# Performance work log

Hardware: AMD Instinct MI355X
Metric: run time of the kernel (lower is better)

Reference implementation:

```python
import jax, jax.numpy as jnp
import numpy as np
import math

L, D, NH, DFF, RPE = 6, 256, 8, 1024, 512
HD = D // NH
B, NQ = 2, 300
FH, FW = 64, 64
N = FH * FW
STRIDE = 16
SCALE = 1.0 / math.sqrt(HD)


def _ln(x, w, b, eps=1e-5):
    m = jnp.mean(x, -1, keepdims=True)
    v = jnp.mean((x - m) ** 2, -1, keepdims=True)
    return (x - m) * jax.lax.rsqrt(v + eps) * w + b


def _mha_self(x, pos, in_w, in_b, out_w, out_b):
    # torch nn.MultiheadAttention with packed in_proj, q=k=x+pos, v=x
    qk = x + pos
    wq, wk, wv = jnp.split(in_w, 3, 0)
    bq, bk, bv = jnp.split(in_b, 3, 0)
    q = (qk @ wq.T + bq).reshape(B, NQ, NH, HD)
    k = (qk @ wk.T + bk).reshape(B, NQ, NH, HD)
    v = (x @ wv.T + bv).reshape(B, NQ, NH, HD)
    a = jax.nn.softmax(jnp.einsum('bqhd,bkhd->bhqk', q, k) * SCALE, -1)
    o = jnp.einsum('bhqk,bkhd->bqhd', a, v).reshape(B, NQ, D)
    return o @ out_w.T + out_b


def _cross(q_in, box, k_in, v_in, qw, qb, kw, kb, vw, vb, pw, pb,
           c1w1, c1b1, c1w2, c2w1, c2b1, c2w2):
    # box: [B,NQ,1,4] xyxy in absolute pixels; learned relative position bias
    pos_x = (jnp.arange(FW, dtype=jnp.float32) + 0.5) * STRIDE  # linspace(0.5,w-0.5,w)*stride
    pos_y = (jnp.arange(FH, dtype=jnp.float32) + 0.5) * STRIDE
    dx = box[..., 0::2] - pos_x[None, None, :, None]  # [B,NQ,FW,2]
    dy = box[..., 1::2] - pos_y[None, None, :, None]  # [B,NQ,FH,2]
    rpe_x = jax.nn.relu(dx @ c1w1.T + c1b1) @ c1w2.T  # [B,NQ,FW,NH]
    rpe_y = jax.nn.relu(dy @ c2w1.T + c2b1) @ c2w2.T  # [B,NQ,FH,NH]
    rpe = (rpe_y[:, :, :, None, :] + rpe_x[:, :, None, :, :]).reshape(B, NQ, N, NH)
    q = ((q_in @ qw.T + qb) * SCALE).reshape(B, NQ, NH, HD)
    k = (k_in @ kw.T + kb).reshape(B, N, NH, HD)
    v = (v_in @ vw.T + vb).reshape(B, N, NH, HD)
    attn = jnp.einsum('bqhd,bkhd->bhqk', q, k) + rpe.transpose(0, 3, 1, 2)
    a = jax.nn.softmax(attn, -1)
    o = jnp.einsum('bhqk,bkhd->bqhd', a, v).reshape(B, NQ, D)
    return o @ pw.T + pb


def _decoder(tgt, query_pos, reference_points, src, src_pos_embed,
             sa_in_w, sa_in_b, sa_out_w, sa_out_b, n1_w, n1_b,
             ca_q_w, ca_q_b, ca_k_w, ca_k_b, ca_v_w, ca_v_b, ca_proj_w, ca_proj_b,
             cpb1_w1, cpb1_b1, cpb1_w2, cpb2_w1, cpb2_b1, cpb2_w2,
             n2_w, n2_b, ffn_w1, ffn_b1, ffn_w2, ffn_b2, n3_w, n3_b):
    ref = reference_points[:, :, None]  # [B,NQ,1,4] cxcywh
    box = jnp.concatenate([ref[..., :2] - ref[..., 2:] * 0.5,
                           ref[..., :2] + ref[..., 2:] * 0.5], -1)
    kv = src + src_pos_embed
    out = tgt
    for i in range(L):  # post-norm decoder layers, dropout=0 (eval)
        t = _mha_self(out, query_pos, sa_in_w[i], sa_in_b[i], sa_out_w[i], sa_out_b[i])
        out = _ln(out + t, n1_w[i], n1_b[i])
        t = _cross(out + query_pos, box, kv, src,
                   ca_q_w[i], ca_q_b[i], ca_k_w[i], ca_k_b[i], ca_v_w[i], ca_v_b[i],
                   ca_proj_w[i], ca_proj_b[i], cpb1_w1[i], cpb1_b1[i], cpb1_w2[i],
                   cpb2_w1[i], cpb2_b1[i], cpb2_w2[i])
        out = _ln(out + t, n2_w[i], n2_b[i])
        t = jax.nn.relu(out @ ffn_w1[i].T + ffn_b1[i]) @ ffn_w2[i].T + ffn_b2[i]
        out = _ln(out + t, n3_w[i], n3_b[i])
    return out


def setup_inputs() -> dict:
    key = jax.random.key(0)
    ks = iter(jax.random.split(key, 64))
    def w(*shape, s=0.02):
        return jax.random.normal(next(ks), shape, jnp.float32) * s
    inp = {}
    inp['tgt'] = w(B, NQ, D, s=1.0)
    inp['query_pos'] = w(B, NQ, D, s=1.0)
    cxcy = jax.random.uniform(next(ks), (B, NQ, 2)) * (FW * STRIDE)
    wh = jax.random.uniform(next(ks), (B, NQ, 2)) * 256.0 + 16.0
    inp['reference_points'] = jnp.concatenate([cxcy, wh], -1)
    inp['src'] = w(B, N, D, s=1.0)
    inp['src_pos_embed'] = w(B, N, D, s=1.0)
    inp['src_spatial_shapes'] = jnp.array([[FH, FW]], jnp.int32)
    inp['sa_in_w'] = w(L, 3 * D, D); inp['sa_in_b'] = jnp.zeros((L, 3 * D))
    inp['sa_out_w'] = w(L, D, D); inp['sa_out_b'] = jnp.zeros((L, D))
    inp['n1_w'] = jnp.ones((L, D)); inp['n1_b'] = jnp.zeros((L, D))
    inp['ca_q_w'] = w(L, D, D); inp['ca_q_b'] = jnp.zeros((L, D))
    inp['ca_k_w'] = w(L, D, D); inp['ca_k_b'] = jnp.zeros((L, D))
    inp['ca_v_w'] = w(L, D, D); inp['ca_v_b'] = jnp.zeros((L, D))
    inp['ca_proj_w'] = w(L, D, D); inp['ca_proj_b'] = jnp.zeros((L, D))
    inp['cpb1_w1'] = w(L, RPE, 2, s=0.001); inp['cpb1_b1'] = jnp.zeros((L, RPE))
    inp['cpb1_w2'] = w(L, NH, RPE, s=0.001)
    inp['cpb2_w1'] = w(L, RPE, 2, s=0.001); inp['cpb2_b1'] = jnp.zeros((L, RPE))
    inp['cpb2_w2'] = w(L, NH, RPE, s=0.001)
    inp['n2_w'] = jnp.ones((L, D)); inp['n2_b'] = jnp.zeros((L, D))
    inp['ffn_w1'] = w(L, DFF, D); inp['ffn_b1'] = jnp.zeros((L, DFF))
    inp['ffn_w2'] = w(L, D, DFF); inp['ffn_b2'] = jnp.zeros((L, D))
    inp['n3_w'] = jnp.ones((L, D)); inp['n3_b'] = jnp.zeros((L, D))
    return inp


def reference(tgt, query_pos, reference_points, src, src_pos_embed, src_spatial_shapes,
              sa_in_w, sa_in_b, sa_out_w, sa_out_b, n1_w, n1_b,
              ca_q_w, ca_q_b, ca_k_w, ca_k_b, ca_v_w, ca_v_b, ca_proj_w, ca_proj_b,
              cpb1_w1, cpb1_b1, cpb1_w2, cpb2_w1, cpb2_b1, cpb2_w2,
              n2_w, n2_b, ffn_w1, ffn_b1, ffn_w2, ffn_b2, n3_w, n3_b):
    # src_spatial_shapes is static ([[FH, FW]]); dims closed over as constants.
    return _decoder(tgt, query_pos, reference_points, src, src_pos_embed,
                    sa_in_w, sa_in_b, sa_out_w, sa_out_b, n1_w, n1_b,
                    ca_q_w, ca_q_b, ca_k_w, ca_k_b, ca_v_w, ca_v_b, ca_proj_w, ca_proj_b,
                    cpb1_w1, cpb1_b1, cpb1_w2, cpb2_w1, cpb2_b1, cpb2_w2,
                    n2_w, n2_b, ffn_w1, ffn_b1, ffn_w2, ffn_b2, n3_w, n3_b)
```

## Files before the change

### kernel.cpp

```cpp
#include <hip/hip_runtime.h>
#include <math.h>

#define NQ   300
#define DMODEL 256
#define NHEAD 8
#define HDIM 32
#define BB   2
#define NKV  4096
#define RPEH 512
#define NLAYER 6
#define ATTN_SCALE 0.17677669529663687f

typedef short short8 __attribute__((ext_vector_type(8)));
typedef float f32x4 __attribute__((ext_vector_type(4)));
typedef unsigned short ushort_t;

__device__ __forceinline__ short f2bf(float f) {
    union { float fv; unsigned u; } v; v.fv = f;
    unsigned r = v.u + 0x7FFFu + ((v.u >> 16) & 1u);
    return (short)(r >> 16);
}
__device__ __forceinline__ float bf2f(ushort_t u) {
    union { unsigned u; float f; } v; v.u = ((unsigned)u) << 16;
    return v.f;
}
__device__ __forceinline__ short8 pack_bf8(float4 x, float4 y) {
    short8 v;
    v[0] = f2bf(x.x); v[1] = f2bf(x.y); v[2] = f2bf(x.z); v[3] = f2bf(x.w);
    v[4] = f2bf(y.x); v[5] = f2bf(y.y); v[6] = f2bf(y.z); v[7] = f2bf(y.w);
    return v;
}

__global__ __launch_bounds__(256) void prep_kernel(
    const float* __restrict__ src, const float* __restrict__ spe,
    const float* __restrict__ tgt, const float* __restrict__ qpos,
    const float* __restrict__ refp,
    ushort_t* __restrict__ kvb16, ushort_t* __restrict__ srcb16,
    float* __restrict__ outb, ushort_t* __restrict__ ob16,
    ushort_t* __restrict__ oq16,
    float* __restrict__ boxx, float* __restrict__ boxy)
{
    int i = blockIdx.x * 256 + threadIdx.x;
    if (i < BB * NKV * DMODEL) {
        float s = src[i];
        kvb16[i]  = (ushort_t)f2bf(s + spe[i]);
        srcb16[i] = (ushort_t)f2bf(s);
    }
    if (i < BB * NQ * DMODEL) {
        float tv = tgt[i];
        outb[i] = tv;
        ob16[i] = (ushort_t)f2bf(tv);
        oq16[i] = (ushort_t)f2bf(tv + qpos[i]);
    }
    if (i < BB * NQ) {
        float cx = refp[i * 4 + 0], cy = refp[i * 4 + 1];
        float w  = refp[i * 4 + 2], h  = refp[i * 4 + 3];
        boxx[i * 2 + 0] = cx - 0.5f * w;
        boxx[i * 2 + 1] = cx + 0.5f * w;
        boxy[i * 2 + 0] = cy - 0.5f * h;
        boxy[i * 2 + 1] = cy + 0.5f * h;
    }
}

__global__ __launch_bounds__(256) void wconv_kernel(
    const float* __restrict__ sain, const float* __restrict__ saout,
    const float* __restrict__ caq, const float* __restrict__ cak,
    const float* __restrict__ cav, const float* __restrict__ cap,
    const float* __restrict__ f1, const float* __restrict__ f2,
    ushort_t* __restrict__ dst)
{
    size_t i = ((size_t)blockIdx.x * 256 + threadIdx.x) * 8;
    if (i >= 6291456) return;
    const float* s; size_t off;
    if      (i < 1179648) { s = sain;  off = i; }
    else if (i < 1572864) { s = saout; off = i - 1179648; }
    else if (i < 1966080) { s = caq;   off = i - 1572864; }
    else if (i < 2359296) { s = cak;   off = i - 1966080; }
    else if (i < 2752512) { s = cav;   off = i - 2359296; }
    else if (i < 3145728) { s = cap;   off = i - 2752512; }
    else if (i < 4718592) { s = f1;    off = i - 3145728; }
    else                  { s = f2;    off = i - 4718592; }
    float4 x = *(const float4*)&s[off];
    float4 y = *(const float4*)&s[off + 4];
    *(short8*)&dst[i] = pack_bf8(x, y);
}

__global__ __launch_bounds__(256) void kv_mega(
    const ushort_t* __restrict__ kvb16, const ushort_t* __restrict__ srcb16,
    const ushort_t* __restrict__ Wk, const ushort_t* __restrict__ Wv,
    const float* __restrict__ kbias, const float* __restrict__ vbias,
    ushort_t* __restrict__ Kcb, ushort_t* __restrict__ Vcb)
{
    __shared__ short A_s[64][264];
    const int t = threadIdx.x;
    const int lane = t & 63, w = t >> 6;
    const int wr = w >> 1, wc = w & 1;
    const int l15 = lane & 15, lhi8 = (lane >> 4) * 8;

    const int wgid = blockIdx.x;
    const int xcd  = wgid & 7;
    const int idx  = wgid >> 3;
    const int n0   = (idx & 3) * 64;
    const int sel  = (idx >> 2) & 1;
    const int m0   = (xcd * 16 + (idx >> 3)) * 64;

    const ushort_t* A  = sel ? srcb16 : kvb16;
    const ushort_t* Wb = sel ? Wv : Wk;
    const float* bb    = sel ? vbias : kbias;
    ushort_t* Cb       = sel ? Vcb : Kcb;

    {
        int row = t >> 2, c0 = (t & 3) * 64;
        const ushort_t* ap = &A[(size_t)(m0 + row) * 256 + c0];
#pragma unroll
        for (int c8 = 0; c8 < 8; ++c8)
            *(short8*)&A_s[row][c0 + c8 * 8] = *(const short8*)(ap + c8 * 8);
    }
    __syncthreads();

    const int ar0 = wr * 32 + l15, ar1 = ar0 + 16;
    const int rowb = m0 + wr * 32 + (lane >> 4) * 4;
    const int colb = n0 + wc * 32 + l15;

    for (int l = 0; l < NLAYER; ++l) {
        const ushort_t* wp0 = &Wb[(size_t)l * 65536 + (size_t)(n0 + wc * 32 + l15) * 256 + lhi8];
        const ushort_t* wp1 = wp0 + 16 * 256;
        f32x4 acc[2][2];
#pragma unroll
        for (int i = 0; i < 2; ++i)
#pragma unroll
            for (int j = 0; j < 2; ++j)
#pragma unroll
                for (int r = 0; r < 4; ++r) acc[i][j][r] = 0.f;
#pragma unroll
        for (int k0 = 0; k0 < 256; k0 += 32) {
            short8 a0 = *(short8*)&A_s[ar0][k0 + lhi8];
            short8 a1 = *(short8*)&A_s[ar1][k0 + lhi8];
            short8 b0 = *(const short8*)(wp0 + k0);
            short8 b1 = *(const short8*)(wp1 + k0);
            acc[0][0] = __builtin_amdgcn_mfma_f32_16x16x32_bf16(a0, b0, acc[0][0], 0, 0, 0);
            acc[0][1] = __builtin_amdgcn_mfma_f32_16x16x32_bf16(a0, b1, acc[0][1], 0, 0, 0);
            acc[1][0] = __builtin_amdgcn_mfma_f32_16x16x32_bf16(a1, b0, acc[1][0], 0, 0, 0);
            acc[1][1] = __builtin_amdgcn_mfma_f32_16x16x32_bf16(a1, b1, acc[1][1], 0, 0, 0);
        }
        ushort_t* C = Cb + (size_t)l * (BB * NKV * DMODEL);
        const float* bl = bb + l * 256;
#pragma unroll
        for (int ni = 0; ni < 2; ++ni) {
            int col = colb + ni * 16;
            float bv = bl[col];
#pragma unroll
            for (int mi = 0; mi < 2; ++mi)
#pragma unroll
                for (int r = 0; r < 4; ++r) {
                    int row = rowb + mi * 16 + r;
                    C[(size_t)row * 256 + col] = (ushort_t)f2bf(acc[mi][ni][r] + bv);
                }
        }
    }
}

template<int OUT_BF16, int RELU>
__global__ __launch_bounds__(256) void gemm_direct(
    const ushort_t* __restrict__ A1, const ushort_t* __restrict__ A2, int plimit,
    int lda, const ushort_t* __restrict__ W, const float* __restrict__ bias,
    void* __restrict__ Cv, int ldc, int M, int K, float scale, int slimit)
{
    const int t = threadIdx.x;
    const int lane = t & 63, w = t >> 6;
    const int wr = w >> 1, wc = w & 1;
    const int l15 = lane & 15, lhi8 = (lane >> 4) * 8;
    const int m0 = blockIdx.y * 64, n0 = blockIdx.x * 64;
    const ushort_t* A = (n0 < plimit) ? A1 : A2;

    int r0 = m0 + wr * 32 + l15;      if (r0 > M - 1) r0 = M - 1;
    int r1 = m0 + wr * 32 + 16 + l15; if (r1 > M - 1) r1 = M - 1;
    const ushort_t* ap0 = &A[(size_t)r0 * lda + lhi8];
    const ushort_t* ap1 = &A[(size_t)r1 * lda + lhi8];
    const ushort_t* wp0 = &W[(size_t)(n0 + wc * 32 + l15) * K + lhi8];
    const ushort_t* wp1 = wp0 + (size_t)16 * K;

    f32x4 acc[2][2];
#pragma unroll
    for (int i = 0; i < 2; ++i)
#pragma unroll
        for (int j = 0; j < 2; ++j)
#pragma unroll
            for (int r = 0; r < 4; ++r) acc[i][j][r] = 0.f;

    for (int k0 = 0; k0 < K; k0 += 32) {
        short8 a0 = *(const short8*)(ap0 + k0);
        short8 a1 = *(const short8*)(ap1 + k0);
        short8 b0 = *(const short8*)(wp0 + k0);
        short8 b1 = *(const short8*)(wp1 + k0);
        acc[0][0] = __builtin_amdgcn_mfma_f32_16x16x32_bf16(a0, b0, acc[0][0], 0, 0, 0);
        acc[0][1] = __builtin_amdgcn_mfma_f32_16x16x32_bf16(a0, b1, acc[0][1], 0, 0, 0);
        acc[1][0] = __builtin_amdgcn_mfma_f32_16x16x32_bf16(a1, b0, acc[1][0], 0, 0, 0);
        acc[1][1] = __builtin_amdgcn_mfma_f32_16x16x32_bf16(a1, b1, acc[1][1], 0, 0, 0);
    }

    const int rowb = m0 + wr * 32 + (lane >> 4) * 4;
    const int colb = n0 + wc * 32 + l15;
#pragma unroll
    for (int ni = 0; ni < 2; ++ni) {
        int col = colb + ni * 16;
        float bv = bias[col];
#pragma unroll
        for (int mi = 0; mi < 2; ++mi)
#pragma unroll
            for (int r = 0; r < 4; ++r) {
                int row = rowb + mi * 16 + r;
                if (row < M) {
                    float v = acc[mi][ni][r] + bv;
                    if (col < slimit) v *= scale;
                    if (RELU) v = fmaxf(v, 0.f);
                    if (OUT_BF16)
                        ((ushort_t*)Cv)[(size_t)row * ldc + col] = (ushort_t)f2bf(v);
                    else
                        ((float*)Cv)[(size_t)row * ldc + col] = v;
                }
            }
    }
}

__global__ __launch_bounds__(256) void ln_residual(
    float* __restrict__ out, const float* __restrict__ tt,
    const float* __restrict__ qpos,
    const float* __restrict__ w, const float* __restrict__ b,
    ushort_t* __restrict__ ob16, ushort_t* __restrict__ oq16, int rows)
{
    const int wid = threadIdx.x >> 6, lane = threadIdx.x & 63;
    const int row = blockIdx.x * 4 + wid;
    if (row >= rows) return;
    const float* orow = out + row * DMODEL;
    const float* trow = tt + row * DMODEL;
    float x[4];
#pragma unroll
    for (int i = 0; i < 4; ++i) x[i] = orow[lane + 64 * i] + trow[lane + 64 * i];
    float s = x[0] + x[1] + x[2] + x[3];
#pragma unroll
    for (int mask = 1; mask < 64; mask <<= 1) s += __shfl_xor(s, mask);
    float mean = s * (1.f / 256.f);
    float vs = 0.f;
#pragma unroll
    for (int i = 0; i < 4; ++i) { float d = x[i] - mean; vs += d * d; }
#pragma unroll
    for (int mask = 1; mask < 64; mask <<= 1) vs += __shfl_xor(vs, mask);
    float r = rsqrtf(vs * (1.f / 256.f) + 1e-5f);
    float* orw = out + row * DMODEL;
#pragma unroll
    for (int i = 0; i < 4; ++i) {
        int c = lane + 64 * i;
        float val = (x[i] - mean) * r * w[c] + b[c];
        orw[c] = val;
        ob16[row * DMODEL + c] = (ushort_t)f2bf(val);
        oq16[row * DMODEL + c] = (ushort_t)f2bf(val + qpos[row * DMODEL + c]);
    }
}

__global__ __launch_bounds__(256) void rpe_all(
    const float* __restrict__ boxx, const float* __restrict__ boxy,
    const float* __restrict__ cpb1_w1, const float* __restrict__ cpb1_b1,
    const float* __restrict__ cpb1_w2,
    const float* __restrict__ cpb2_w1, const float* __restrict__ cpb2_b1,
    const float* __restrict__ cpb2_w2,
    float* __restrict__ rx6, float* __restrict__ ry6)
{
    __shared__ __align__(16) float2 as2_s[RPEH];
    __shared__ short w2b_s[8][520];

    const int bq = blockIdx.x;
    const int axis = blockIdx.y;
    const int l = blockIdx.z;
    const float* __restrict__ w1 = (axis ? cpb2_w1 : cpb1_w1) + (size_t)l * 1024;
    const float* __restrict__ b1 = (axis ? cpb2_b1 : cpb1_b1) + (size_t)l * 512;
    const float* __restrict__ w2 = (axis ? cpb2_w2 : cpb1_w2) + (size_t)l * 4096;
    const float* __restrict__ bx = axis ? boxy : boxx;
    const int t = threadIdx.x;

    const float x0 = bx[bq * 2 + 0], x1 = bx[bq * 2 + 1];

    for (int j = t; j < RPEH; j += 256) {
        float2 wp = *(const float2*)&w1[2 * j];
        as2_s[j] = make_float2(fmaf(wp.x, x0, fmaf(wp.y, x1, b1[j])),
                               wp.x + wp.y);
    }
    {
        int h = t >> 5, j16 = (t & 31) * 16;
        const float* wp = &w2[h * RPEH + j16];
        float4 a = *(const float4*)wp;
        float4 b = *(const float4*)(wp + 4);
        float4 c = *(const float4*)(wp + 8);
        float4 d = *(const float4*)(wp + 12);
        *(short8*)&w2b_s[h][j16]     = pack_bf8(a, b);
        *(short8*)&w2b_s[h][j16 + 8] = pack_bf8(c, d);
    }
    __syncthreads();

    const int lane = t & 63, w = t >> 6;
    const int l15 = lane & 15, lhi8 = (lane >> 4) * 8, lhi4 = (lane >> 4) * 4;
    const float pos_i = ((w * 16 + l15) + 0.5f) * 16.0f;

    f32x4 acc;
#pragma unroll
    for (int r = 0; r < 4; ++r) acc[r] = 0.f;

#pragma unroll 4
    for (int k0 = 0; k0 < RPEH; k0 += 32) {
        const int j0 = k0 + lhi8;
        const float4* ap = (const float4*)&as2_s[j0];
        float4 p0 = ap[0], p1 = ap[1], p2 = ap[2], p3 = ap[3];
        short8 ha;
        ha[0] = f2bf(fmaxf(fmaf(-pos_i, p0.y, p0.x), 0.f));
        ha[1] = f2bf(fmaxf(fmaf(-pos_i, p0.w, p0.z), 0.f));
        ha[2] = f2bf(fmaxf(fmaf(-pos_i, p1.y, p1.x), 0.f));
        ha[3] = f2bf(fmaxf(fmaf(-pos_i, p1.w, p1.z), 0.f));
        ha[4] = f2bf(fmaxf(fmaf(-pos_i, p2.y, p2.x), 0.f));
        ha[5] = f2bf(fmaxf(fmaf(-pos_i, p2.w, p2.z), 0.f));
        ha[6] = f2bf(fmaxf(fmaf(-pos_i, p3.y, p3.x), 0.f));
        ha[7] = f2bf(fmaxf(fmaf(-pos_i, p3.w, p3.z), 0.f));
        short8 wb;
        if (l15 < 8) wb = *(short8*)&w2b_s[l15][j0];
        else { short8 z = {0,0,0,0,0,0,0,0}; wb = z; }
        acc = __builtin_amdgcn_mfma_f32_16x16x32_bf16(ha, wb, acc, 0, 0, 0);
    }

    if (l15 < 8) {
        const int b = bq / NQ, q = bq % NQ;
        float* __restrict__ dst = (axis ? ry6 : rx6) + (size_t)l * 307200;
        float* p = &dst[((size_t)(b * NHEAD + l15) * NQ + q) * 64 + w * 16 + lhi4];
        *(float4*)p = *(float4*)&acc;
    }
}

template<int HAS_RPE>
__global__ __launch_bounds__(256) void attn_mfma(
    const ushort_t* __restrict__ Q, int ldq,
    const ushort_t* __restrict__ K, int ldk,
    const ushort_t* __restrict__ V, int ldv,
    int nkeys, int kps,
    const float* __restrict__ RX, const float* __restrict__ RY,
    ushort_t* __restrict__ po, float* __restrict__ pm, float* __restrict__ pl,
    int nsplit)
{
    __shared__ short Q_s[64][40];
    __shared__ short K_s[64][40];
    __shared__ short V_s[32][72];
    __shared__ short P_s[4][16][72];

    const int t = threadIdx.x;
    const int lane = t & 63, w = t >> 6;
    const int l15 = lane & 15, lhi8 = (lane >> 4) * 8, lhi4 = (lane >> 4) * 4;
    const int bh = blockIdx.y, b = bh >> 3, h = bh & 7;
    const int q0 = blockIdx.x * 64;
    const int sp = blockIdx.z;

    {
        int q = t >> 2, kc = (t & 3) * 8;
        int qi = q0 + q;
        short8 qv = {0,0,0,0,0,0,0,0};
        if (qi < NQ) qv = *(const short8*)&Q[((size_t)(b * NQ + qi)) * ldq + h * HDIM + kc];
        *(short8*)&Q_s[q][kc] = qv;
    }

    float rxv[4][4];
    const float* ryp[4];
    if (HAS_RPE) {
#pragma unroll
        for (int r = 0; r < 4; ++r) {
            int qi = q0 + w * 16 + lhi4 + r;
            int qc = qi < NQ ? qi : NQ - 1;
            const float* rxp = &RX[((size_t)bh * NQ + qc) * 64];
            ryp[r] = &RY[((size_t)bh * NQ + qc) * 64];
#pragma unroll
            for (int nf = 0; nf < 4; ++nf) rxv[r][nf] = rxp[nf * 16 + l15];
        }
    }

    float m_r[4], l_r[4];
    f32x4 oacc[2];
#pragma unroll
    for (int r = 0; r < 4; ++r) { m_r[r] = -1e30f; l_r[r] = 0.f; }
#pragma unroll
    for (int ni = 0; ni < 2; ++ni)
#pragma unroll
        for (int r = 0; r < 4; ++r) oacc[ni][r] = 0.f;

    const int nt = kps >> 6;
    for (int kt = 0; kt < nt; ++kt) {
        const int key0 = sp * kps + (kt << 6);
        __syncthreads();
        {
            int key = t >> 2, kc = (t & 3) * 8;
            int rk = key0 + key;
            int rkc = rk < nkeys ? rk : nkeys - 1;
            short8 kvv = *(const short8*)&K[((size_t)(b * nkeys + rkc)) * ldk + h * HDIM + kc];
            *(short8*)&K_s[key][kc] = kvv;
            short8 vvv = *(const short8*)&V[((size_t)(b * nkeys + rkc)) * ldv + h * HDIM + kc];
#pragma unroll
            for (int j = 0; j < 8; ++j) V_s[kc + j][key] = vvv[j];
        }
        __syncthreads();

        short8 aq = *(short8*)&Q_s[w * 16 + l15][lhi8];
        f32x4 sacc[4];
#pragma unroll
        for (int nf = 0; nf < 4; ++nf) {
#pragma unroll
            for (int r = 0; r < 4; ++r) sacc[nf][r] = 0.f;
            short8 kb = *(short8*)&K_s[nf * 16 + l15][lhi8];
            sacc[nf] = __builtin_amdgcn_mfma_f32_16x16x32_bf16(aq, kb, sacc[nf], 0, 0, 0);
        }

        const int ktg = key0 >> 6;
        const bool kv0 = key0 +      l15 < nkeys;
        const bool kv1 = key0 + 16 + l15 < nkeys;
        const bool kv2 = key0 + 32 + l15 < nkeys;
        const bool kv3 = key0 + 48 + l15 < nkeys;
        float c_r[4];
#pragma unroll
        for (int r = 0; r < 4; ++r) {
            float ryv = HAS_RPE ? ryp[r][ktg] : 0.f;
            float sv0 = sacc[0][r] + ryv, sv1 = sacc[1][r] + ryv;
            float sv2 = sacc[2][r] + ryv, sv3 = sacc[3][r] + ryv;
            if (HAS_RPE) {
                sv0 += rxv[r][0]; sv1 += rxv[r][1];
                sv2 += rxv[r][2]; sv3 += rxv[r][3];
            }
            sv0 = kv0 ? sv0 : -1e30f;
            sv1 = kv1 ? sv1 : -1e30f;
            sv2 = kv2 ? sv2 : -1e30f;
            sv3 = kv3 ? sv3 : -1e30f;
            float tmax = fmaxf(fmaxf(sv0, sv1), fmaxf(sv2, sv3));
#pragma unroll
            for (int mask = 1; mask < 16; mask <<= 1)
                tmax = fmaxf(tmax, __shfl_xor(tmax, mask));
            float mn = fmaxf(m_r[r], tmax);
            float cc = __expf(m_r[r] - mn);
            m_r[r] = mn; c_r[r] = cc;
            float p0 = __expf(sv0 - mn), p1 = __expf(sv1 - mn);
            float p2 = __expf(sv2 - mn), p3 = __expf(sv3 - mn);
            float ps = p0 + p1 + p2 + p3;
#pragma unroll
            for (int mask = 1; mask < 16; mask <<= 1) ps += __shfl_xor(ps, mask);
            l_r[r] = l_r[r] * cc + ps;
            P_s[w][lhi4 + r][     l15] = f2bf(p0);
            P_s[w][lhi4 + r][16 + l15] = f2bf(p1);
            P_s[w][lhi4 + r][32 + l15] = f2bf(p2);
            P_s[w][lhi4 + r][48 + l15] = f2bf(p3);
        }
#pragma unroll
        for (int ni = 0; ni < 2; ++ni)
#pragma unroll
            for (int r = 0; r < 4; ++r) oacc[ni][r] *= c_r[r];

        short8 pa0 = *(short8*)&P_s[w][l15][lhi8];
        short8 pa1 = *(short8*)&P_s[w][l15][32 + lhi8];
#pragma unroll
        for (int ni = 0; ni < 2; ++ni) {
            short8 vb0 = *(short8*)&V_s[ni * 16 + l15][lhi8];
            short8 vb1 = *(short8*)&V_s[ni * 16 + l15][32 + lhi8];
            oacc[ni] = __builtin_amdgcn_mfma_f32_16x16x32_bf16(pa0, vb0, oacc[ni], 0, 0, 0);
            oacc[ni] = __builtin_amdgcn_mfma_f32_16x16x32_bf16(pa1, vb1, oacc[ni], 0, 0, 0);
        }
    }

#pragma unroll
    for (int r = 0; r < 4; ++r) {
        int qi = q0 + w * 16 + lhi4 + r;
        if (qi < NQ) {
            size_t base = ((size_t)(bh * nsplit + sp) * NQ + qi);
            if (l15 == 0) { pm[base] = m_r[r]; pl[base] = l_r[r]; }
            po[base * 32 + l15] = (ushort_t)f2bf(oacc[0][r]);
            po[base * 32 + 16 + l15] = (ushort_t)f2bf(oacc[1][r]);
        }
    }
}

__global__ __launch_bounds__(256) void combine_gemm(
    const ushort_t* __restrict__ po, const float* __restrict__ pm,
    const float* __restrict__ pl, int nsplit,
    const ushort_t* __restrict__ W, const float* __restrict__ bias,
    float* __restrict__ C, int M)
{
    __shared__ short A_s2[64][264];
    const int t = threadIdx.x;
    const int m0 = blockIdx.y * 64, n0 = blockIdx.x * 64;

    {
        int rloc = t >> 2;
        int row = m0 + rloc;
        int dc = (t & 3) * 64;
        if (row < M) {
            int b = row / NQ, q = row % NQ;
#pragma unroll
            for (int hh = 0; hh < 2; ++hh) {
                int h = (dc >> 5) + hh;
                int bh = b * NHEAD + h;
                float Mx = -1e30f;
                for (int s = 0; s < nsplit; ++s)
                    Mx = fmaxf(Mx, pm[(size_t)(bh * nsplit + s) * NQ + q]);
                float L = 0.f;
                float acc1[32];
#pragma unroll
                for (int d = 0; d < 32; ++d) acc1[d] = 0.f;
                for (int s = 0; s < nsplit; ++s) {
                    size_t base = (size_t)(bh * nsplit + s) * NQ + q;
                    float wgt = __expf(pm[base] - Mx);
                    L += pl[base] * wgt;
                    const ushort_t* pp = &po[base * 32];
#pragma unroll
                    for (int d = 0; d < 32; ++d) acc1[d] += bf2f(pp[d]) * wgt;
                }
                float inv = 1.f / L;
#pragma unroll
                for (int d = 0; d < 32; ++d)
                    A_s2[rloc][dc + hh * 32 + d] = f2bf(acc1[d] * inv);
            }
        } else {
#pragma unroll
            for (int d = 0; d < 64; ++d) A_s2[rloc][dc + d] = 0;
        }
    }
    __syncthreads();

    const int lane = t & 63, w = t >> 6;
    const int wr = w >> 1, wc = w & 1;
    const int l15 = lane & 15, lhi8 = (lane >> 4) * 8;
    const ushort_t* wp0 = &W[(size_t)(n0 + wc * 32 + l15) * 256 + lhi8];
    const ushort_t* wp1 = wp0 + 16 * 256;
    f32x4 acc[2][2];
#pragma unroll
    for (int i = 0; i < 2; ++i)
#pragma unroll
        for (int j = 0; j < 2; ++j)
#pragma unroll
            for (int r = 0; r < 4; ++r) acc[i][j][r] = 0.f;

#pragma unroll
    for (int k0 = 0; k0 < 256; k0 += 32) {
        short8 a0 = *(short8*)&A_s2[wr * 32 + l15][k0 + lhi8];
        short8 a1 = *(short8*)&A_s2[wr * 32 + 16 + l15][k0 + lhi8];
        short8 b0 = *(const short8*)(wp0 + k0);
        short8 b1 = *(const short8*)(wp1 + k0);
        acc[0][0] = __builtin_amdgcn_mfma_f32_16x16x32_bf16(a0, b0, acc[0][0], 0, 0, 0);
        acc[0][1] = __builtin_amdgcn_mfma_f32_16x16x32_bf16(a0, b1, acc[0][1], 0, 0, 0);
        acc[1][0] = __builtin_amdgcn_mfma_f32_16x16x32_bf16(a1, b0, acc[1][0], 0, 0, 0);
        acc[1][1] = __builtin_amdgcn_mfma_f32_16x16x32_bf16(a1, b1, acc[1][1], 0, 0, 0);
    }

    const int rowb = m0 + wr * 32 + (lane >> 4) * 4;
    const int colb = n0 + wc * 32 + l15;
#pragma unroll
    for (int ni = 0; ni < 2; ++ni) {
        int col = colb + ni * 16;
        float bv = bias[col];
#pragma unroll
        for (int mi = 0; mi < 2; ++mi)
#pragma unroll
            for (int r = 0; r < 4; ++r) {
                int row = rowb + mi * 16 + r;
                if (row < M)
                    C[(size_t)row * 256 + col] = acc[mi][ni][r] + bv;
            }
    }
}

extern "C" void kernel_launch(void* const* d_in, const int* in_sizes, int n_in,
                              void* d_out, int out_size, void* d_ws, size_t ws_size,
                              hipStream_t stream)
{
    const float* tgt   = (const float*)d_in[0];
    const float* qpos  = (const float*)d_in[1];
    const float* refp  = (const float*)d_in[2];
    const float* src   = (const float*)d_in[3];
    const float* spe   = (const float*)d_in[4];
    const float* sa_in_w  = (const float*)d_in[6];
    const float* sa_in_b  = (const float*)d_in[7];
    const float* sa_out_w = (const float*)d_in[8];
    const float* sa_out_b = (const float*)d_in[9];
    const float* n1_w  = (const float*)d_in[10];
    const float* n1_b  = (const float*)d_in[11];
    const float* ca_q_w = (const float*)d_in[12];
    const float* ca_q_b = (const float*)d_in[13];
    const float* ca_k_w = (const float*)d_in[14];
    const float* ca_k_b = (const float*)d_in[15];
    const float* ca_v_w = (const float*)d_in[16];
    const float* ca_v_b = (const float*)d_in[17];
    const float* ca_p_w = (const float*)d_in[18];
    const float* ca_p_b = (const float*)d_in[19];
    const float* cpb1_w1 = (const float*)d_in[20];
    const float* cpb1_b1 = (const float*)d_in[21];
    const float* cpb1_w2 = (const float*)d_in[22];
    const float* cpb2_w1 = (const float*)d_in[23];
    const float* cpb2_b1 = (const float*)d_in[24];
    const float* cpb2_w2 = (const float*)d_in[25];
    const float* n2_w = (const float*)d_in[26];
    const float* n2_b = (const float*)d_in[27];
    const float* ffn_w1 = (const float*)d_in[28];
    const float* ffn_b1 = (const float*)d_in[29];
    const float* ffn_w2 = (const float*)d_in[30];
    const float* ffn_b2 = (const float*)d_in[31];
    const float* n3_w = (const float*)d_in[32];
    const float* n3_b = (const float*)d_in[33];

    float* ws  = (float*)d_ws;
    float* outb = ws;
    float* tb   = outb + 153600;
    float* rx6  = tb + 153600;
    float* ry6  = rx6 + 1843200;
    float* boxx = ry6 + 1843200;
    float* boxy = boxx + 1200;
    float* pm   = boxy + 1200;
    float* pl   = pm + 38400;
    ushort_t* u = (ushort_t*)(pl + 38400);
    ushort_t* qkvb   = u;
    ushort_t* qcb    = qkvb + 460800;
    ushort_t* ob16   = qcb + 153600;
    ushort_t* oq16   = ob16 + 153600;
    ushort_t* hbb    = oq16 + 153600;
    ushort_t* poh    = hbb + 614400;
    ushort_t* kvb16  = poh + 1228800;
    ushort_t* srcb16 = kvb16 + 2097152;
    ushort_t* Kcb    = srcb16 + 2097152;
    ushort_t* Vcb    = Kcb + 12582912;
    ushort_t* Wseg   = Vcb + 12582912;
    ushort_t* Wsain  = Wseg;
    ushort_t* Wsaout = Wsain + 1179648;
    ushort_t* Wcaq   = Wsaout + 393216;
    ushort_t* Wcak   = Wcaq + 393216;
    ushort_t* Wcav   = Wcak + 393216;
    ushort_t* Wcap   = Wcav + 393216;
    ushort_t* Wff1   = Wcap + 393216;
    ushort_t* Wff2   = Wff1 + 1572864;

    const int M = BB * NQ;

    prep_kernel<<<8192, 256, 0, stream>>>(src, spe, tgt, qpos, refp,
        kvb16, srcb16, outb, ob16, oq16, boxx, boxy);
    wconv_kernel<<<3072, 256, 0, stream>>>(sa_in_w, sa_out_w, ca_q_w, ca_k_w,
        ca_v_w, ca_p_w, ffn_w1, ffn_w2, Wseg);
    rpe_all<<<dim3(600, 2, 6), 256, 0, stream>>>(boxx, boxy,
        cpb1_w1, cpb1_b1, cpb1_w2, cpb2_w1, cpb2_b1, cpb2_w2, rx6, ry6);
    kv_mega<<<1024, 256, 0, stream>>>(kvb16, srcb16, Wcak, Wcav,
        ca_k_b, ca_v_b, Kcb, Vcb);

    for (int l = 0; l < NLAYER; ++l) {
        gemm_direct<1,0><<<dim3(12, 10), 256, 0, stream>>>(
            oq16, ob16, 512, 256, Wsain + (size_t)l * 196608, sa_in_b + (size_t)l * 768,
            qkvb, 768, M, 256, ATTN_SCALE, 256);
        attn_mfma<0><<<dim3(5, 16, 5), 256, 0, stream>>>(
            qkvb, 768, qkvb + 256, 768, qkvb + 512, 768,
            NQ, 64, nullptr, nullptr, poh, pm, pl, 5);
        combine_gemm<<<dim3(4, 10), 256, 0, stream>>>(
            poh, pm, pl, 5, Wsaout + (size_t)l * 65536, sa_out_b + l * 256, tb, M);
        ln_residual<<<150, 256, 0, stream>>>(outb, tb, qpos,
            n1_w + l * 256, n1_b + l * 256, ob16, oq16, M);

        gemm_direct<1,0><<<dim3(4, 10), 256, 0, stream>>>(
            oq16, oq16, 256, 256, Wcaq + (size_t)l * 65536, ca_q_b + l * 256,
            qcb, 256, M, 256, ATTN_SCALE, 256);
        attn_mfma<1><<<dim3(5, 16, 8), 256, 0, stream>>>(
            qcb, 256, Kcb + (size_t)l * 2097152, 256, Vcb + (size_t)l * 2097152, 256,
            NKV, 512, rx6 + (size_t)l * 307200, ry6 + (size_t)l * 307200,
            poh, pm, pl, 8);
        combine_gemm<<<dim3(4, 10), 256, 0, stream>>>(
            poh, pm, pl, 8, Wcap + (size_t)l * 65536, ca_p_b + l * 256, tb, M);
        ln_residual<<<150, 256, 0, stream>>>(outb, tb, qpos,
            n2_w + l * 256, n2_b + l * 256, ob16, oq16, M);

        gemm_direct<1,1><<<dim3(16, 10), 256, 0, stream>>>(
            ob16, ob16, 1024, 256, Wff1 + (size_t)l * 262144, ffn_b1 + l * 1024,
            hbb, 1024, M, 256, 1.f, 0);
        gemm_direct<0,0><<<dim3(4, 10), 256, 0, stream>>>(
            hbb, hbb, 256, 1024, Wff2 + (size_t)l * 262144, ffn_b2 + l * 256,
            tb, 256, M, 1024, 1.f, 0);
        ln_residual<<<150, 256, 0, stream>>>(outb, tb, qpos,
            n3_w + l * 256, n3_b + l * 256, ob16, oq16, M);
    }

    hipMemcpyAsync(d_out, outb, (size_t)M * DMODEL * sizeof(float),
                   hipMemcpyDeviceToDevice, stream);
}
```

Before: 778.0 us.

## Double cross-attention KV splits and load kv_mega A operands into registers

The cross-attention split-KV kernel now uses 16 splits of 256 keys instead of 8 of 512, doubling the grid, and the combine GEMM merges 16 partials. Workspace for the partial max/sum and partial outputs is enlarged to match. The aim is more workgroups to fill the GPU during cross-attention, at the cost of more partial-result traffic and combine work. Separately, kv_mega drops its LDS staging and barrier, loading A fragments straight from global memory into registers. That raises register pressure.

```diff
diff --git a/kernel.cpp b/kernel.cpp
--- a/kernel.cpp
+++ b/kernel.cpp
@@ -91,7 +91,6 @@
     const float* __restrict__ kbias, const float* __restrict__ vbias,
     ushort_t* __restrict__ Kcb, ushort_t* __restrict__ Vcb)
 {
-    __shared__ short A_s[64][264];
     const int t = threadIdx.x;
     const int lane = t & 63, w = t >> 6;
     const int wr = w >> 1, wc = w & 1;
@@ -109,16 +108,15 @@
     const float* bb    = sel ? vbias : kbias;
     ushort_t* Cb       = sel ? Vcb : Kcb;
 
-    {
-        int row = t >> 2, c0 = (t & 3) * 64;
-        const ushort_t* ap = &A[(size_t)(m0 + row) * 256 + c0];
-#pragma unroll
-        for (int c8 = 0; c8 < 8; ++c8)
-            *(short8*)&A_s[row][c0 + c8 * 8] = *(const short8*)(ap + c8 * 8);
-    }
-    __syncthreads();
-
-    const int ar0 = wr * 32 + l15, ar1 = ar0 + 16;
+    const ushort_t* ap0 = &A[(size_t)(m0 + wr * 32 + l15) * 256 + lhi8];
+    const ushort_t* ap1 = ap0 + 16 * 256;
+    short8 a0r[8], a1r[8];
+#pragma unroll
+    for (int k = 0; k < 8; ++k) {
+        a0r[k] = *(const short8*)(ap0 + k * 32);
+        a1r[k] = *(const short8*)(ap1 + k * 32);
+    }
+
     const int rowb = m0 + wr * 32 + (lane >> 4) * 4;
     const int colb = n0 + wc * 32 + l15;
 
@@ -133,15 +131,13 @@
 #pragma unroll
                 for (int r = 0; r < 4; ++r) acc[i][j][r] = 0.f;
 #pragma unroll
-        for (int k0 = 0; k0 < 256; k0 += 32) {
-            short8 a0 = *(short8*)&A_s[ar0][k0 + lhi8];
-            short8 a1 = *(short8*)&A_s[ar1][k0 + lhi8];
-            short8 b0 = *(const short8*)(wp0 + k0);
-            short8 b1 = *(const short8*)(wp1 + k0);
-            acc[0][0] = __builtin_amdgcn_mfma_f32_16x16x32_bf16(a0, b0, acc[0][0], 0, 0, 0);
-            acc[0][1] = __builtin_amdgcn_mfma_f32_16x16x32_bf16(a0, b1, acc[0][1], 0, 0, 0);
-            acc[1][0] = __builtin_amdgcn_mfma_f32_16x16x32_bf16(a1, b0, acc[1][0], 0, 0, 0);
-            acc[1][1] = __builtin_amdgcn_mfma_f32_16x16x32_bf16(a1, b1, acc[1][1], 0, 0, 0);
+        for (int k = 0; k < 8; ++k) {
+            short8 b0 = *(const short8*)(wp0 + k * 32);
+            short8 b1 = *(const short8*)(wp1 + k * 32);
+            acc[0][0] = __builtin_amdgcn_mfma_f32_16x16x32_bf16(a0r[k], b0, acc[0][0], 0, 0, 0);
+            acc[0][1] = __builtin_amdgcn_mfma_f32_16x16x32_bf16(a0r[k], b1, acc[0][1], 0, 0, 0);
+            acc[1][0] = __builtin_amdgcn_mfma_f32_16x16x32_bf16(a1r[k], b0, acc[1][0], 0, 0, 0);
+            acc[1][1] = __builtin_amdgcn_mfma_f32_16x16x32_bf16(a1r[k], b1, acc[1][1], 0, 0, 0);
         }
         ushort_t* C = Cb + (size_t)l * (BB * NKV * DMODEL);
         const float* bl = bb + l * 256;
@@ -612,15 +608,15 @@
     float* boxx = ry6 + 1843200;
     float* boxy = boxx + 1200;
     float* pm   = boxy + 1200;
-    float* pl   = pm + 38400;
-    ushort_t* u = (ushort_t*)(pl + 38400);
+    float* pl   = pm + 76800;
+    ushort_t* u = (ushort_t*)(pl + 76800);
     ushort_t* qkvb   = u;
     ushort_t* qcb    = qkvb + 460800;
     ushort_t* ob16   = qcb + 153600;
     ushort_t* oq16   = ob16 + 153600;
     ushort_t* hbb    = oq16 + 153600;
     ushort_t* poh    = hbb + 614400;
-    ushort_t* kvb16  = poh + 1228800;
+    ushort_t* kvb16  = poh + 2457600;
     ushort_t* srcb16 = kvb16 + 2097152;
     ushort_t* Kcb    = srcb16 + 2097152;
     ushort_t* Vcb    = Kcb + 12582912;
@@ -660,12 +656,12 @@
         gemm_direct<1,0><<<dim3(4, 10), 256, 0, stream>>>(
             oq16, oq16, 256, 256, Wcaq + (size_t)l * 65536, ca_q_b + l * 256,
             qcb, 256, M, 256, ATTN_SCALE, 256);
-        attn_mfma<1><<<dim3(5, 16, 8), 256, 0, stream>>>(
+        attn_mfma<1><<<dim3(5, 16, 16), 256, 0, stream>>>(
             qcb, 256, Kcb + (size_t)l * 2097152, 256, Vcb + (size_t)l * 2097152, 256,
-            NKV, 512, rx6 + (size_t)l * 307200, ry6 + (size_t)l * 307200,
-            poh, pm, pl, 8);
+            NKV, 256, rx6 + (size_t)l * 307200, ry6 + (size_t)l * 307200,
+            poh, pm, pl, 16);
         combine_gemm<<<dim3(4, 10), 256, 0, stream>>>(
-            poh, pm, pl, 8, Wcap + (size_t)l * 65536, ca_p_b + l * 256, tb, M);
+            poh, pm, pl, 16, Wcap + (size_t)l * 65536, ca_p_b + l * 256, tb, M);
         ln_residual<<<150, 256, 0, stream>>>(outb, tb, qpos,
             n2_w + l * 256, n2_b + l * 256, ob16, oq16, M);
 
```

Result: slower. 817.7 us (+5.1%).
